# Kernel tuning notes

Measured on AMD Instinct MI355X. Metric: run time of the kernel, lower is better.

## Reference

```python
import jax, jax.numpy as jnp
import numpy as np

N_TH1 = 25
LB = 1e-20
UB = 1e20
LB_EXP = -20.0


def _make_directions(n_th1):
    # Spherical direction grid exactly as in the TF __init__ (interior ring points, then 2 poles).
    n_th2 = 2 * (n_th1 - 1) + 1
    th1 = np.linspace(-np.pi / 2, np.pi / 2, n_th1)
    th2 = np.linspace(-np.pi, np.pi, n_th2)
    c1, s1 = np.cos(th1), np.sin(th1)
    c2, s2 = np.cos(th2), np.sin(th2)
    i = np.arange(1, n_th1 - 1)
    j = np.arange(0, n_th2 - 1)
    C1 = c1[i][:, None]
    dx = (C1 * c2[j][None, :]).ravel()
    dy = (C1 * s2[j][None, :]).ravel()
    dz = np.broadcast_to(s1[i][:, None], (len(i), len(j))).ravel()
    d = np.stack([dx, dy, dz], axis=-1)
    poles = np.array([[c1[0] * c2[0], c1[0] * s2[0], s1[0]],
                      [c1[-1] * c2[0], c1[-1] * s2[0], s1[-1]]])
    return np.concatenate([d, poles], axis=0).astype(np.float32)  # [n_dirs, 3]


def setup_inputs():
    key = jax.random.key(0)
    k1, k2 = jax.random.split(key)
    B, P, V = 8, 32, 256
    vertices = jax.random.normal(k1, (B, P, V, 3), dtype=jnp.float32)
    # smoothness p in [2, 20] (power-mean exponent must be > 1 for meaningful support fn)
    smoothness = jax.random.uniform(k2, (B, P), dtype=jnp.float32) * 18.0 + 2.0
    directions = jnp.asarray(_make_directions(N_TH1))  # [1106, 3]
    return {"vertices": vertices, "smoothness": smoothness, "directions": directions}


def _forward(vertices, smoothness, directions):
    B, P, V, _ = vertices.shape
    D = directions.shape[0]
    mean_vertices = jnp.mean(vertices, axis=2, keepdims=True)          # [B,P,1,3]
    local_vertices = vertices - mean_vertices                          # [B,P,V,3]

    # z[b,p,v,d] = <local_vertex, direction>
    z = jnp.einsum('bpvc,dc->bpvd', local_vertices, directions)        # [B,P,V,D]
    zm = jnp.where(z > 0, z, 0.0)                                      # relu, == cast(z>0)*z
    p = smoothness[:, :, None, None]                                   # [B,P,1,1]

    # dynamic rescaling exponent k = 10^ceil(max(0, (-20 - p*log10(max_v zm)) / p))
    safe_zm = jnp.where(zm > 0, zm, 1.0)
    zm_log = jnp.max(jnp.where(zm > 0, jnp.log(safe_zm) / jnp.log(10.0), -jnp.inf),
                     axis=2, keepdims=True)                            # [B,P,1,D]
    exponent = zm_log * p
    lk = jnp.where(exponent < LB_EXP, (LB_EXP - exponent) / p, 0.0)
    k = jnp.power(10.0, jnp.clip(jnp.ceil(lk), 0.0, UB))               # [B,P,1,D]
    k = jax.lax.stop_gradient(k)  # ceil has zero grad in TF too

    zms = zm * k                                                       # [B,P,V,D]
    # zm^p, with exact-zero entries mapped back to 0 (clip(0^p)=LB then -LB in TF)
    safe_zms = jnp.where(zms > 0, zms, 1.0)
    zm_p = jnp.where(zms > 0, jnp.clip(jnp.power(safe_zms, p), LB, UB), 0.0)
    sum_zm_p = jnp.sum(zm_p, axis=2, keepdims=True)                    # [B,P,1,D]
    h = jnp.clip(jnp.power(sum_zm_p, 1.0 / p), LB, UB)                 # [B,P,1,D]

    # dh/dz = clip((zm_scaled / h)^(p-1)); TF keeps the LB floor here (no subtraction)
    ratio = zms / h
    safe_ratio = jnp.where(ratio > 0, ratio, 1.0)
    dhdz = jnp.where(ratio > 0, jnp.clip(jnp.power(safe_ratio, p - 1.0), LB, UB), LB)

    # surface points s = (dh/dz)^T V + t
    surf = jnp.einsum('bpvd,bpvc->bpdc', dhdz, local_vertices) + mean_vertices  # [B,P,D,3]

    h_out = jnp.transpose(h / k, (0, 1, 3, 2))                         # [B,P,D,1]
    local_dirs = jnp.broadcast_to(directions[None, None], (B, P, D, 3))
    direction_h = jnp.concatenate([local_dirs, h_out], axis=-1)        # [B,P,D,4]

    points = surf.reshape(B, P * D, 3)
    mean_v = mean_vertices.reshape(B, P, 3)
    zeros = jnp.zeros((1, 1, 1, 1), jnp.float32)
    return (points, direction_h, mean_v, directions, local_vertices, zeros, zeros)


def reference(vertices, smoothness, directions):
    return _forward(vertices, smoothness, directions)
```

## Files before the change

kernel.cpp:

```cpp
#include <hip/hip_runtime.h>
#include <math.h>

#define BLOCK 256
#define LBv 1e-20f
#define UBv 1e20f

#if __has_builtin(__builtin_amdgcn_logf) && __has_builtin(__builtin_amdgcn_exp2f)
__device__ __forceinline__ float fast_log2(float x) { return __builtin_amdgcn_logf(x); }
__device__ __forceinline__ float fast_exp2(float x) { return __builtin_amdgcn_exp2f(x); }
#else
__device__ __forceinline__ float fast_log2(float x) { return log2f(x); }
__device__ __forceinline__ float fast_exp2(float x) { return exp2f(x); }
#endif

__global__ __launch_bounds__(BLOCK) void mcnet_sreg(
    const float* __restrict__ verts,
    const float* __restrict__ smooth,
    const float* __restrict__ dirs,
    float* __restrict__ out,
    int NT, int V, int D, int SPLIT,
    size_t offDH, size_t offMV, size_t offDIR, size_t offLV, size_t offZ)
{
    __shared__ float red[3 * BLOCK];

    const int tid  = threadIdx.x;
    const int tile = blockIdx.x / SPLIT;
    const int s    = blockIdx.x % SPLIT;

    const float* vp0 = verts + (size_t)tile * V * 3;

    float sx = 0.f, sy = 0.f, sz = 0.f;
    for (int v = tid; v < V; v += BLOCK) {
        sx += vp0[3 * v + 0]; sy += vp0[3 * v + 1]; sz += vp0[3 * v + 2];
    }
    red[tid] = sx; red[tid + BLOCK] = sy; red[tid + 2 * BLOCK] = sz;
    __syncthreads();
    for (int st = BLOCK / 2; st > 0; st >>= 1) {
        if (tid < st) {
            red[tid]             += red[tid + st];
            red[tid + BLOCK]     += red[tid + BLOCK + st];
            red[tid + 2 * BLOCK] += red[tid + 2 * BLOCK + st];
        }
        __syncthreads();
    }
    const float inv = 1.0f / (float)V;
    const float mx = red[0] * inv, my = red[BLOCK] * inv, mz = red[2 * BLOCK] * inv;

    if (s == 0) {
        for (int v = tid; v < V; v += BLOCK) {
            size_t o = offLV + ((size_t)tile * V + v) * 3;
            out[o + 0] = vp0[3 * v + 0] - mx;
            out[o + 1] = vp0[3 * v + 1] - my;
            out[o + 2] = vp0[3 * v + 2] - mz;
        }
        if (tid == 0) {
            size_t mo = offMV + (size_t)tile * 3;
            out[mo + 0] = mx;
            out[mo + 1] = my;
            out[mo + 2] = mz;
        }
    }
    if (blockIdx.x == 0) {
        for (int i = tid; i < D * 3; i += BLOCK)
            out[offDIR + i] = dirs[i];
        if (tid < 2) out[offZ + tid] = 0.f;
    }

    const int d = s * BLOCK + tid;
    if (d >= D) return;

    const float dx = dirs[d * 3 + 0];
    const float dy = dirs[d * 3 + 1];
    const float dz = dirs[d * 3 + 2];
    const float pv = smooth[tile];
    const float c1 = pv - 1.f;
    const float Sthresh = (float)V * 1e-10f;

    const float nmd = -(mx * dx + my * dy + mz * dz);

    float S = 0.f, Wx = 0.f, Wy = 0.f, Wz = 0.f, Ws = 0.f;
    #pragma unroll 8
    for (int v = 0; v < V; ++v) {
        float vx = vp0[3 * v + 0];
        float vy = vp0[3 * v + 1];
        float vz = vp0[3 * v + 2];
        float z  = fmaf(vx, dx, fmaf(vy, dy, fmaf(vz, dz, nmd)));
        float zc = fmaxf(z, 0.f);
        float l  = fast_log2(zc);
        float w  = fast_exp2(c1 * l);
        S  = fmaf(w, zc, S);
        Wx = fmaf(w, vx, Wx);
        Wy = fmaf(w, vy, Wy);
        Wz = fmaf(w, vz, Wz);
        Ws += w;
    }

    size_t po  = ((size_t)tile * D + d) * 3;
    size_t dho = offDH + ((size_t)tile * D + d) * 4;

    if (S >= Sthresh) {
        float h = fminf(fmaxf(fast_exp2(fast_log2(S) * (1.f / pv)), LBv), UBv);
        float scale = fast_exp2(-c1 * fast_log2(h));
        float ax = fmaf(-mx, Ws, Wx);
        float ay = fmaf(-my, Ws, Wy);
        float az = fmaf(-mz, Ws, Wz);
        out[po + 0] = fmaf(ax, scale, mx);
        out[po + 1] = fmaf(ay, scale, my);
        out[po + 2] = fmaf(az, scale, mz);
        out[dho + 0] = dx;
        out[dho + 1] = dy;
        out[dho + 2] = dz;
        out[dho + 3] = h;
    } else {
        float zmax = 0.f;
        for (int v = 0; v < V; ++v) {
            float z = fmaf(vp0[3 * v] - mx, dx,
                      fmaf(vp0[3 * v + 1] - my, dy, (vp0[3 * v + 2] - mz) * dz));
            zmax = fmaxf(zmax, z);
        }
        float zm_log   = (zmax > 0.f) ? log10f(zmax) : -INFINITY;
        float exponent = zm_log * pv;
        float lk = (exponent < -20.f) ? (-20.f - exponent) / pv : 0.f;
        float kk = powf(10.f, fminf(fmaxf(ceilf(lk), 0.f), UBv));

        float sum = 0.f;
        for (int v = 0; v < V; ++v) {
            float z = fmaf(vp0[3 * v] - mx, dx,
                      fmaf(vp0[3 * v + 1] - my, dy, (vp0[3 * v + 2] - mz) * dz));
            float zms = fmaxf(z, 0.f) * kk;
            float w   = (zms > 0.f) ? fminf(fmaxf(powf(zms, pv), LBv), UBv) : 0.f;
            sum += w;
        }
        float h = fminf(fmaxf(powf(sum, 1.f / pv), LBv), UBv);

        float bx = 0.f, by = 0.f, bz = 0.f;
        for (int v = 0; v < V; ++v) {
            float lx = vp0[3 * v] - mx, ly = vp0[3 * v + 1] - my, lz = vp0[3 * v + 2] - mz;
            float z     = fmaf(lx, dx, fmaf(ly, dy, lz * dz));
            float zms   = fmaxf(z, 0.f) * kk;
            float ratio = zms / h;
            float w = (ratio > 0.f) ? fminf(fmaxf(powf(ratio, c1), LBv), UBv) : LBv;
            bx = fmaf(w, lx, bx);
            by = fmaf(w, ly, by);
            bz = fmaf(w, lz, bz);
        }
        out[po + 0] = bx + mx;
        out[po + 1] = by + my;
        out[po + 2] = bz + mz;
        out[dho + 0] = dx;
        out[dho + 1] = dy;
        out[dho + 2] = dz;
        out[dho + 3] = h / kk;
    }
}

extern "C" void kernel_launch(void* const* d_in, const int* in_sizes, int n_in,
                              void* d_out, int out_size, void* d_ws, size_t ws_size,
                              hipStream_t stream) {
    const float* verts  = (const float*)d_in[0];
    const float* smooth = (const float*)d_in[1];
    const float* dirs   = (const float*)d_in[2];
    float* out = (float*)d_out;

    const int NT = in_sizes[1];
    const int D  = in_sizes[2] / 3;
    const int V  = in_sizes[0] / (3 * NT);
    const int SPLIT = (D + BLOCK - 1) / BLOCK;

    const size_t offDH  = (size_t)NT * D * 3;
    const size_t offMV  = offDH  + (size_t)NT * D * 4;
    const size_t offDIR = offMV  + (size_t)NT * 3;
    const size_t offLV  = offDIR + (size_t)D * 3;
    const size_t offZ   = offLV  + (size_t)NT * V * 3;

    dim3 grid(NT * SPLIT);
    dim3 block(BLOCK);
    hipLaunchKernelGGL(mcnet_sreg, grid, block, 0, stream,
                       verts, smooth, dirs, out,
                       NT, V, D, SPLIT, offDH, offMV, offDIR, offLV, offZ);
}
```

Measured before the change: 91.80 us.

## Split vertex reduction across two blocks with separate epilogue kernel

Each tile/direction-chunk block now handles only half of the vertices and writes five partial sums to workspace. A second kernel adds the halves and computes h, the surface points and the rare slow-path fallback. This doubles grid parallelism to improve latency hiding. In exchange it adds a second launch, workspace traffic, and a redundant per-block mean reduction.

```diff
diff --git a/kernel.cpp b/kernel.cpp
--- a/kernel.cpp
+++ b/kernel.cpp
@@ -13,19 +13,23 @@
 __device__ __forceinline__ float fast_exp2(float x) { return exp2f(x); }
 #endif
 
-__global__ __launch_bounds__(BLOCK) void mcnet_sreg(
+__global__ __launch_bounds__(BLOCK) void mcnet_partial(
     const float* __restrict__ verts,
     const float* __restrict__ smooth,
     const float* __restrict__ dirs,
     float* __restrict__ out,
+    float* __restrict__ ws5,
+    float* __restrict__ wsM,
     int NT, int V, int D, int SPLIT,
-    size_t offDH, size_t offMV, size_t offDIR, size_t offLV, size_t offZ)
+    size_t offMV, size_t offDIR, size_t offLV, size_t offZ)
 {
     __shared__ float red[3 * BLOCK];
 
     const int tid  = threadIdx.x;
-    const int tile = blockIdx.x / SPLIT;
-    const int s    = blockIdx.x % SPLIT;
+    const int half = blockIdx.x & 1;
+    const int rest = blockIdx.x >> 1;
+    const int tile = rest / SPLIT;
+    const int s    = rest % SPLIT;
 
     const float* vp0 = verts + (size_t)tile * V * 3;
 
@@ -46,7 +50,7 @@
     const float inv = 1.0f / (float)V;
     const float mx = red[0] * inv, my = red[BLOCK] * inv, mz = red[2 * BLOCK] * inv;
 
-    if (s == 0) {
+    if (s == 0 && half == 0) {
         for (int v = tid; v < V; v += BLOCK) {
             size_t o = offLV + ((size_t)tile * V + v) * 3;
             out[o + 0] = vp0[3 * v + 0] - mx;
@@ -55,9 +59,8 @@
         }
         if (tid == 0) {
             size_t mo = offMV + (size_t)tile * 3;
-            out[mo + 0] = mx;
-            out[mo + 1] = my;
-            out[mo + 2] = mz;
+            out[mo + 0] = mx; out[mo + 1] = my; out[mo + 2] = mz;
+            wsM[tile * 3 + 0] = mx; wsM[tile * 3 + 1] = my; wsM[tile * 3 + 2] = mz;
         }
     }
     if (blockIdx.x == 0) {
@@ -74,13 +77,14 @@
     const float dz = dirs[d * 3 + 2];
     const float pv = smooth[tile];
     const float c1 = pv - 1.f;
-    const float Sthresh = (float)V * 1e-10f;
-
     const float nmd = -(mx * dx + my * dy + mz * dz);
+
+    const int v0 = half * (V >> 1);
+    const int v1 = half ? V : (V >> 1);
 
     float S = 0.f, Wx = 0.f, Wy = 0.f, Wz = 0.f, Ws = 0.f;
     #pragma unroll 8
-    for (int v = 0; v < V; ++v) {
+    for (int v = v0; v < v1; ++v) {
         float vx = vp0[3 * v + 0];
         float vy = vp0[3 * v + 1];
         float vz = vp0[3 * v + 2];
@@ -95,8 +99,51 @@
         Ws += w;
     }
 
-    size_t po  = ((size_t)tile * D + d) * 3;
-    size_t dho = offDH + ((size_t)tile * D + d) * 4;
+    const size_t NTD = (size_t)NT * D;
+    const size_t gid = (size_t)tile * D + d;
+    float* base = ws5 + (size_t)half * 5 * NTD + gid;
+    base[0 * NTD] = S;
+    base[1 * NTD] = Wx;
+    base[2 * NTD] = Wy;
+    base[3 * NTD] = Wz;
+    base[4 * NTD] = Ws;
+}
+
+__global__ __launch_bounds__(BLOCK) void mcnet_epilogue(
+    const float* __restrict__ verts,
+    const float* __restrict__ smooth,
+    const float* __restrict__ dirs,
+    float* __restrict__ out,
+    const float* __restrict__ ws5,
+    const float* __restrict__ wsM,
+    int NT, int V, int D, size_t offDH)
+{
+    const size_t NTD = (size_t)NT * D;
+    const size_t gid = (size_t)blockIdx.x * BLOCK + threadIdx.x;
+    if (gid >= NTD) return;
+
+    const int tile = (int)(gid / D);
+    const int d    = (int)(gid - (size_t)tile * D);
+
+    const float S  = ws5[0 * NTD + gid] + ws5[5 * NTD + gid];
+    const float Wx = ws5[1 * NTD + gid] + ws5[6 * NTD + gid];
+    const float Wy = ws5[2 * NTD + gid] + ws5[7 * NTD + gid];
+    const float Wz = ws5[3 * NTD + gid] + ws5[8 * NTD + gid];
+    const float Ws = ws5[4 * NTD + gid] + ws5[9 * NTD + gid];
+
+    const float mx = wsM[tile * 3 + 0];
+    const float my = wsM[tile * 3 + 1];
+    const float mz = wsM[tile * 3 + 2];
+
+    const float dx = dirs[d * 3 + 0];
+    const float dy = dirs[d * 3 + 1];
+    const float dz = dirs[d * 3 + 2];
+    const float pv = smooth[tile];
+    const float c1 = pv - 1.f;
+    const float Sthresh = (float)V * 1e-10f;
+
+    size_t po  = gid * 3;
+    size_t dho = offDH + gid * 4;
 
     if (S >= Sthresh) {
         float h = fminf(fmaxf(fast_exp2(fast_log2(S) * (1.f / pv)), LBv), UBv);
@@ -112,6 +159,7 @@
         out[dho + 2] = dz;
         out[dho + 3] = h;
     } else {
+        const float* vp0 = verts + (size_t)tile * V * 3;
         float zmax = 0.f;
         for (int v = 0; v < V; ++v) {
             float z = fmaf(vp0[3 * v] - mx, dx,
@@ -166,16 +214,25 @@
     const int D  = in_sizes[2] / 3;
     const int V  = in_sizes[0] / (3 * NT);
     const int SPLIT = (D + BLOCK - 1) / BLOCK;
-
-    const size_t offDH  = (size_t)NT * D * 3;
-    const size_t offMV  = offDH  + (size_t)NT * D * 4;
+    const size_t NTD = (size_t)NT * D;
+
+    const size_t offDH  = NTD * 3;
+    const size_t offMV  = offDH  + NTD * 4;
     const size_t offDIR = offMV  + (size_t)NT * 3;
     const size_t offLV  = offDIR + (size_t)D * 3;
     const size_t offZ   = offLV  + (size_t)NT * V * 3;
 
-    dim3 grid(NT * SPLIT);
+    float* ws5 = (float*)d_ws;
+    float* wsM = ws5 + 10 * NTD;
+
     dim3 block(BLOCK);
-    hipLaunchKernelGGL(mcnet_sreg, grid, block, 0, stream,
-                       verts, smooth, dirs, out,
-                       NT, V, D, SPLIT, offDH, offMV, offDIR, offLV, offZ);
+    dim3 gridA(NT * SPLIT * 2);
+    hipLaunchKernelGGL(mcnet_partial, gridA, block, 0, stream,
+                       verts, smooth, dirs, out, ws5, wsM,
+                       NT, V, D, SPLIT, offMV, offDIR, offLV, offZ);
+
+    dim3 gridB((unsigned)((NTD + BLOCK - 1) / BLOCK));
+    hipLaunchKernelGGL(mcnet_epilogue, gridB, block, 0, stream,
+                       verts, smooth, dirs, out, ws5, wsM,
+                       NT, V, D, offDH);
 }
```

New measurement: 96.25 us. +4.8%, slower.

## Split vertex loop across two block halves with shared-memory partial reduction

Applied to the files above, without the earlier changes.

Each block now covers 128 directions instead of 256, with the two halves of the block each summing over half of the vertices and combining partial sums through shared memory. This doubles the grid size, halves the serial per-thread loop length and reduces padded direction slots. It adds a block barrier, shared-memory traffic and more blocks that redundantly recompute the per-tile vertex mean.

```diff
diff --git a/kernel.cpp b/kernel.cpp
--- a/kernel.cpp
+++ b/kernel.cpp
@@ -2,6 +2,7 @@
 #include <math.h>
 
 #define BLOCK 256
+#define DPB   128
 #define LBv 1e-20f
 #define UBv 1e20f
 
@@ -13,7 +14,7 @@
 __device__ __forceinline__ float fast_exp2(float x) { return exp2f(x); }
 #endif
 
-__global__ __launch_bounds__(BLOCK) void mcnet_sreg(
+__global__ __launch_bounds__(BLOCK) void mcnet_vsplit(
     const float* __restrict__ verts,
     const float* __restrict__ smooth,
     const float* __restrict__ dirs,
@@ -55,9 +56,7 @@
         }
         if (tid == 0) {
             size_t mo = offMV + (size_t)tile * 3;
-            out[mo + 0] = mx;
-            out[mo + 1] = my;
-            out[mo + 2] = mz;
+            out[mo + 0] = mx; out[mo + 1] = my; out[mo + 2] = mz;
         }
     }
     if (blockIdx.x == 0) {
@@ -66,21 +65,26 @@
         if (tid < 2) out[offZ + tid] = 0.f;
     }
 
-    const int d = s * BLOCK + tid;
-    if (d >= D) return;
-
-    const float dx = dirs[d * 3 + 0];
-    const float dy = dirs[d * 3 + 1];
-    const float dz = dirs[d * 3 + 2];
+    const int slot = tid & (DPB - 1);
+    const int half = tid >> 7;
+    const int d    = s * DPB + slot;
+    const bool active = (d < D);
+    const int dc   = active ? d : (D - 1);
+
+    const float dx = dirs[dc * 3 + 0];
+    const float dy = dirs[dc * 3 + 1];
+    const float dz = dirs[dc * 3 + 2];
     const float pv = smooth[tile];
     const float c1 = pv - 1.f;
-    const float Sthresh = (float)V * 1e-10f;
-
     const float nmd = -(mx * dx + my * dy + mz * dz);
+
+    const int vh = V >> 1;
+    const int v0 = half ? vh : 0;
+    const int v1 = half ? V : vh;
 
     float S = 0.f, Wx = 0.f, Wy = 0.f, Wz = 0.f, Ws = 0.f;
     #pragma unroll 8
-    for (int v = 0; v < V; ++v) {
+    for (int v = v0; v < v1; ++v) {
         float vx = vp0[3 * v + 0];
         float vy = vp0[3 * v + 1];
         float vz = vp0[3 * v + 2];
@@ -95,6 +99,24 @@
         Ws += w;
     }
 
+    __syncthreads();
+    if (half) {
+        red[slot + 0 * DPB] = S;
+        red[slot + 1 * DPB] = Wx;
+        red[slot + 2 * DPB] = Wy;
+        red[slot + 3 * DPB] = Wz;
+        red[slot + 4 * DPB] = Ws;
+    }
+    __syncthreads();
+    if (half || !active) return;
+
+    S  += red[slot + 0 * DPB];
+    Wx += red[slot + 1 * DPB];
+    Wy += red[slot + 2 * DPB];
+    Wz += red[slot + 3 * DPB];
+    Ws += red[slot + 4 * DPB];
+
+    const float Sthresh = (float)V * 1e-10f;
     size_t po  = ((size_t)tile * D + d) * 3;
     size_t dho = offDH + ((size_t)tile * D + d) * 4;
 
@@ -165,17 +187,18 @@
     const int NT = in_sizes[1];
     const int D  = in_sizes[2] / 3;
     const int V  = in_sizes[0] / (3 * NT);
-    const int SPLIT = (D + BLOCK - 1) / BLOCK;
-
-    const size_t offDH  = (size_t)NT * D * 3;
-    const size_t offMV  = offDH  + (size_t)NT * D * 4;
+    const int SPLIT = (D + DPB - 1) / DPB;
+
+    const size_t NTD = (size_t)NT * D;
+    const size_t offDH  = NTD * 3;
+    const size_t offMV  = offDH  + NTD * 4;
     const size_t offDIR = offMV  + (size_t)NT * 3;
     const size_t offLV  = offDIR + (size_t)D * 3;
     const size_t offZ   = offLV  + (size_t)NT * V * 3;
 
     dim3 grid(NT * SPLIT);
     dim3 block(BLOCK);
-    hipLaunchKernelGGL(mcnet_sreg, grid, block, 0, stream,
+    hipLaunchKernelGGL(mcnet_vsplit, grid, block, 0, stream,
                        verts, smooth, dirs, out,
                        NT, V, D, SPLIT, offDH, offMV, offDIR, offLV, offZ);
 }
```

After: 92.18 us. No clear change (+0.4%).
